# Kernel optimization log

Measured on AMD Instinct MI355X. Metric: run time of the kernel, lower is better.

Reference implementation:

```python
import jax, jax.numpy as jnp
import numpy as np

DEPTH = 2
D_MODEL = 768
D_STATE = 64
EXPAND = 2
D_CONV = 4
D_INNER = EXPAND * D_MODEL          # 1536
DT_RANK = (D_MODEL + 15) // 16      # 48
BATCH, SEQ = 4, 2048


def setup_inputs() -> dict:
    key = jax.random.key(0)
    ks = jax.random.split(key, 8)
    s = 0.02  # small init scale for stability
    return {
        "x": jax.random.normal(ks[0], (BATCH, SEQ, D_MODEL), jnp.float32),
        # per-layer params stacked along leading DEPTH axis
        "in_proj_w": jax.random.normal(ks[1], (DEPTH, 2 * D_INNER, D_MODEL), jnp.float32) * s,
        "conv_w": jax.random.normal(ks[2], (DEPTH, D_INNER, D_CONV), jnp.float32) * s,
        "conv_b": jnp.zeros((DEPTH, D_INNER), jnp.float32),
        "x_proj_w": jax.random.normal(ks[3], (DEPTH, DT_RANK + 2 * D_STATE, D_INNER), jnp.float32) * s,
        "dt_proj_w": jax.random.normal(ks[4], (DEPTH, D_INNER, DT_RANK), jnp.float32) * s,
        "dt_proj_b": jax.random.normal(ks[5], (DEPTH, D_INNER), jnp.float32) * s,
        # S4D-real init: A = -[1..N] per channel -> A_log = log(arange)
        "A_log": jnp.tile(jnp.log(jnp.arange(1, D_STATE + 1, dtype=jnp.float32))[None, None, :],
                          (DEPTH, D_INNER, 1)),
        "D_skip": jnp.ones((DEPTH, D_INNER), jnp.float32),
        "out_proj_w": jax.random.normal(ks[6], (DEPTH, D_MODEL, D_INNER), jnp.float32) * s,
    }


def _causal_conv1d(x, w, b):
    # depthwise causal conv: x [B,L,d], w [d,K], b [d]
    L = x.shape[1]
    xp = jnp.pad(x, ((0, 0), (D_CONV - 1, 0), (0, 0)))
    y = b
    for k in range(D_CONV):
        y = y + xp[:, k:k + L, :] * w[:, k]
    return y


def _selective_scan(u, dt, A, Bm, Cm):
    # u, dt: [B,L,d]; A: [d,N]; Bm, Cm: [B,L,N]
    def step(h, inp):
        dt_t, B_t, C_t, u_t = inp  # [B,d],[B,N],[B,N],[B,d]
        dA = jnp.exp(dt_t[..., None] * A)                         # [B,d,N]
        h = dA * h + dt_t[..., None] * B_t[:, None, :] * u_t[..., None]
        y_t = jnp.einsum('bdn,bn->bd', h, C_t)
        return h, y_t

    h0 = jnp.zeros((u.shape[0], u.shape[2], A.shape[1]), u.dtype)
    xs = (jnp.swapaxes(dt, 0, 1), jnp.swapaxes(Bm, 0, 1),
          jnp.swapaxes(Cm, 0, 1), jnp.swapaxes(u, 0, 1))
    _, ys = jax.lax.scan(step, h0, xs)  # ys [L,B,d]
    return jnp.swapaxes(ys, 0, 1)


def _mamba_layer(x, Wi, cw, cb, Wx, Wdt, bdt, A_log, Dp, Wo):
    xz = x @ Wi.T                                  # [B,L,2*d_inner]
    xpart, z = jnp.split(xz, 2, axis=-1)
    xpart = jax.nn.silu(_causal_conv1d(xpart, cw, cb))
    xdbl = xpart @ Wx.T                            # [B,L,dt_rank+2N]
    dt_in, Bm, Cm = jnp.split(xdbl, [DT_RANK, DT_RANK + D_STATE], axis=-1)
    dt = jax.nn.softplus(dt_in @ Wdt.T + bdt)      # [B,L,d_inner]
    A = -jnp.exp(A_log)                            # [d_inner, N]
    y = _selective_scan(xpart, dt, A, Bm, Cm) + Dp * xpart
    y = y * jax.nn.silu(z)
    return y @ Wo.T                                # [B,L,d_model]


def reference(x, in_proj_w, conv_w, conv_b, x_proj_w, dt_proj_w, dt_proj_b,
              A_log, D_skip, out_proj_w):
    for i in range(DEPTH):
        x = _mamba_layer(x, in_proj_w[i], conv_w[i], conv_b[i], x_proj_w[i],
                         dt_proj_w[i], dt_proj_b[i], A_log[i], D_skip[i],
                         out_proj_w[i])
    return x
```

## Files before the change

kernel.cpp:

```cpp
#include <hip/hip_runtime.h>
#include <hip/hip_bf16.h>
#include <math.h>

#define DEPTH   2
#define DM      768
#define DS      64
#define DC      4
#define DI      1536
#define DTR     48
#define BATCH   4
#define SEQ     2048
#define MROWS   (BATCH*SEQ)
#define XDC     (DTR + 2*DS)
#define NC      8
#define TCH     (SEQ/NC)
#define LOG2E   1.44269504088896f

typedef __attribute__((ext_vector_type(8))) short bf16x8;
typedef __attribute__((ext_vector_type(4))) float f32x4;
typedef __attribute__((ext_vector_type(2))) float f32x2;
typedef __attribute__((ext_vector_type(2))) unsigned int uint2v;
typedef unsigned short ushort_t;
#define GAS __attribute__((address_space(1)))
#define LAS __attribute__((address_space(3)))

__device__ __forceinline__ float silu_fast(float x) {
    return x / (1.f + __expf(-x));
}
__device__ __forceinline__ float softplus_acc(float x) {
    return x > 20.f ? x : log1pf(expf(x));
}

__device__ __forceinline__ ushort_t bf16_hi(float f) {
    unsigned u = __float_as_uint(f);
    unsigned hr = u + 0x7FFF + ((u >> 16) & 1);
    return (ushort_t)(hr >> 16);
}

__device__ __forceinline__ f32x2 merge_x32_2(f32x2 a, f32x2 b) {
#if __has_builtin(__builtin_amdgcn_permlane32_swap)
    const uint2v rx = __builtin_amdgcn_permlane32_swap(
        __float_as_uint(a.x), __float_as_uint(b.x), false, false);
    const uint2v ry = __builtin_amdgcn_permlane32_swap(
        __float_as_uint(a.y), __float_as_uint(b.y), false, false);
    const f32x2 s0 = {__uint_as_float(rx[0]), __uint_as_float(ry[0])};
    const f32x2 s1 = {__uint_as_float(rx[1]), __uint_as_float(ry[1])};
    return s0 + s1;
#else
    const f32x2 sa = {a.x + __shfl_xor(a.x, 32, 64), a.y + __shfl_xor(a.y, 32, 64)};
    const f32x2 sb = {b.x + __shfl_xor(b.x, 32, 64), b.y + __shfl_xor(b.y, 32, 64)};
    return (threadIdx.x & 32) ? sb : sa;
#endif
}

__device__ __forceinline__ f32x2 merge_x16_2(f32x2 a, f32x2 b) {
#if __has_builtin(__builtin_amdgcn_permlane16_swap)
    const uint2v rx = __builtin_amdgcn_permlane16_swap(
        __float_as_uint(a.x), __float_as_uint(b.x), false, false);
    const uint2v ry = __builtin_amdgcn_permlane16_swap(
        __float_as_uint(a.y), __float_as_uint(b.y), false, false);
    const f32x2 s0 = {__uint_as_float(rx[0]), __uint_as_float(ry[0])};
    const f32x2 s1 = {__uint_as_float(rx[1]), __uint_as_float(ry[1])};
    return s0 + s1;
#else
    const f32x2 sa = {a.x + __shfl_xor(a.x, 16, 64), a.y + __shfl_xor(a.y, 16, 64)};
    const f32x2 sb = {b.x + __shfl_xor(b.x, 16, 64), b.y + __shfl_xor(b.y, 16, 64)};
    return (threadIdx.x & 16) ? sb : sa;
#endif
}

template <int CTRL>
__device__ __forceinline__ f32x2 dpp_add2(f32x2 x) {
    const int tx = __builtin_amdgcn_update_dpp(
        0, __float_as_int(x.x), CTRL, 0xF, 0xF, true);
    const int ty = __builtin_amdgcn_update_dpp(
        0, __float_as_int(x.y), CTRL, 0xF, 0xF, true);
    const f32x2 t = {__int_as_float(tx), __int_as_float(ty)};
    return x + t;
}
__device__ __forceinline__ f32x2 rowsum16_2(f32x2 x) {
    x = dpp_add2<0x128>(x);
    x = dpp_add2<0x124>(x);
    x = dpp_add2<0x122>(x);
    x = dpp_add2<0x121>(x);
    return x;
}

__global__ __launch_bounds__(256) void quant_bf16(
    const float* __restrict__ in, ushort_t* __restrict__ hi)
{
    const size_t i = ((size_t)blockIdx.x * 256 + threadIdx.x) * 4;
    const float4 v = *(const float4*)(in + i);
    ushort4 h;
    h.x = bf16_hi(v.x); h.y = bf16_hi(v.y);
    h.z = bf16_hi(v.z); h.w = bf16_hi(v.w);
    *(ushort4*)(hi + i) = h;
}

__global__ __launch_bounds__(256, 2) void gemm_mfma(
    const ushort_t* __restrict__ A, const ushort_t* __restrict__ W,
    float* __restrict__ C, int N, int K, int ldA, int ldW,
    ushort_t* __restrict__ Chi, float4* __restrict__ bc4out, int mode)
{
    __shared__ ushort_t lds[2][128 * 32];
    const int tid  = threadIdx.x;
    const int wave = tid >> 6, lane = tid & 63;

    int bx = blockIdx.x, by = blockIdx.y;
    {
        const int X   = gridDim.x;
        const int fid = by * X + bx;
        const int xcd = fid & 7;
        const int j   = fid >> 3;
        const int jX  = j / X;
        by = xcd * (gridDim.y >> 3) + jX;
        bx = j - jX * X;
    }
    const int bm0 = by * 128, bn0 = bx * 128;
    const int wm = (wave >> 1) * 64, wn = (wave & 1) * 64;

    const int srow = lane >> 2;
    const int skq  = (lane & 3) * 8;

    f32x4 acc[4][4];
#pragma unroll
    for (int i = 0; i < 4; i++)
#pragma unroll
        for (int j = 0; j < 4; j++) acc[i][j] = (f32x4){0.f, 0.f, 0.f, 0.f};

    const int lm  = lane & 15;
    const int kg8 = (lane >> 4) * 8;

    for (int k0 = 0; k0 < K; k0 += 32) {
#pragma unroll
        for (int j = 0; j < 4; j++) {
            const int ldid = wave * 4 + j;
            const int buf  = ldid >> 3;
            const int slot = ldid & 7;
            const ushort_t* gsrc = buf ? W : A;
            const int ldg = buf ? ldW : ldA;
            const int rb  = buf ? bn0 : bm0;
            const ushort_t* ga = gsrc + (size_t)(rb + slot * 16 + srow) * ldg + k0 + skq;
            __builtin_amdgcn_global_load_lds(
                (const GAS unsigned*)ga, (LAS unsigned*)&lds[buf][slot * 512], 16, 0, 0);
        }
        __syncthreads();

        bf16x8 ah[4], bh[4];
#pragma unroll
        for (int i = 0; i < 4; i++) {
            const int ar = (wm + i * 16 + lm) * 32 + kg8;
            ah[i] = *(const bf16x8*)&lds[0][ar];
            const int br = (wn + i * 16 + lm) * 32 + kg8;
            bh[i] = *(const bf16x8*)&lds[1][br];
        }
#pragma unroll
        for (int mi = 0; mi < 4; mi++)
#pragma unroll
            for (int ni = 0; ni < 4; ni++)
                acc[mi][ni] = __builtin_amdgcn_mfma_f32_16x16x32_bf16(
                    ah[mi], bh[ni], acc[mi][ni], 0, 0, 0);
        __syncthreads();
    }

#pragma unroll
    for (int mi = 0; mi < 4; mi++)
#pragma unroll
        for (int ni = 0; ni < 4; ni++) {
            const int rowb = bm0 + wm + mi * 16 + (lane >> 4) * 4;
            const int colg = bn0 + wn + ni * 16 + lm;
            if (mode == 1) {
#pragma unroll
                for (int r = 0; r < 4; r++)
                    Chi[(size_t)(rowb + r) * N + colg] = bf16_hi(acc[mi][ni][r]);
            } else if (mode == 2) {
                if (colg >= DTR && colg < DTR + 2 * DS) {
                    const f32x4 a = acc[mi][ni];
                    bc4out[(size_t)(rowb >> 2) * 128 + (colg - DTR)] =
                        make_float4(a[0], a[1], a[2], a[3]);
                } else if (colg < DTR) {
#pragma unroll
                    for (int r = 0; r < 4; r++)
                        C[(size_t)(rowb + r) * N + colg] = acc[mi][ni][r];
                }
            } else {
#pragma unroll
                for (int r = 0; r < 4; r++)
                    if (colg < N)
                        C[(size_t)(rowb + r) * N + colg] = acc[mi][ni][r];
            }
        }
}

__global__ __launch_bounds__(256, 2) void gemm_dt_T(
    const float* __restrict__ Wdt, const float* __restrict__ xdbl,
    const float* __restrict__ bias, float* __restrict__ dtT)
{
    __shared__ float As[8][132];
    __shared__ float Bs[8][132];
    const int tid = threadIdx.x;
    const int bd0 = blockIdx.y * 128;
    const int bt0 = blockIdx.x * 128;
    const int b   = blockIdx.z;
    const int tx = tid & 15;
    const int ty = tid >> 4;
    const int lrow = tid >> 1;
    const int lk4  = (tid & 1) * 4;

    float acc[8][8];
#pragma unroll
    for (int i = 0; i < 8; i++)
#pragma unroll
        for (int j = 0; j < 8; j++) acc[i][j] = 0.f;

    for (int k0 = 0; k0 < DTR; k0 += 8) {
        const float4 av = *(const float4*)(Wdt + (size_t)(bd0 + lrow) * DTR + k0 + lk4);
        const float4 wv = *(const float4*)(xdbl + ((size_t)b * SEQ + bt0 + lrow) * XDC + k0 + lk4);
        __syncthreads();
        As[lk4 + 0][lrow] = av.x; As[lk4 + 1][lrow] = av.y;
        As[lk4 + 2][lrow] = av.z; As[lk4 + 3][lrow] = av.w;
        Bs[lk4 + 0][lrow] = wv.x; Bs[lk4 + 1][lrow] = wv.y;
        Bs[lk4 + 2][lrow] = wv.z; Bs[lk4 + 3][lrow] = wv.w;
        __syncthreads();
#pragma unroll
        for (int kk = 0; kk < 8; kk++) {
            const float4 a0 = *(const float4*)&As[kk][ty * 8];
            const float4 a1 = *(const float4*)&As[kk][ty * 8 + 4];
            const float4 b0 = *(const float4*)&Bs[kk][tx * 8];
            const float4 b1 = *(const float4*)&Bs[kk][tx * 8 + 4];
            const float ar[8] = {a0.x, a0.y, a0.z, a0.w, a1.x, a1.y, a1.z, a1.w};
            const float br[8] = {b0.x, b0.y, b0.z, b0.w, b1.x, b1.y, b1.z, b1.w};
#pragma unroll
            for (int i = 0; i < 8; i++)
#pragma unroll
                for (int j = 0; j < 8; j++)
                    acc[i][j] = fmaf(ar[i], br[j], acc[i][j]);
        }
    }

#pragma unroll
    for (int i = 0; i < 8; i++) {
        const int d = bd0 + ty * 8 + i;
        const float bb = bias[d];
#pragma unroll
        for (int j4 = 0; j4 < 8; j4 += 4) {
            float4 v = make_float4(acc[i][j4], acc[i][j4 + 1], acc[i][j4 + 2], acc[i][j4 + 3]);
            v.x = softplus_acc(v.x + bb);
            v.y = softplus_acc(v.y + bb);
            v.z = softplus_acc(v.z + bb);
            v.w = softplus_acc(v.w + bb);
            *(float4*)(dtT + ((size_t)b * DI + d) * SEQ + bt0 + tx * 8 + j4) = v;
        }
    }
}

__global__ __launch_bounds__(256) void conv_silu_T2(
    const float* __restrict__ xz, const float* __restrict__ cw,
    const float* __restrict__ cb, float* __restrict__ uT,
    ushort_t* __restrict__ uh)
{
    __shared__ float tin[67][65];
    __shared__ float ttr[64][65];
    const int tid = threadIdx.x;
    const int d0 = blockIdx.x * 64, t0 = blockIdx.y * 64, b = blockIdx.z;
    const int cl = tid & 63, q = tid >> 6;

    for (int r = q; r < 67; r += 4) {
        const int t = t0 - 3 + r;
        float v = 0.f;
        if (t >= 0) v = xz[((size_t)b * SEQ + t) * (2 * DI) + d0 + cl];
        tin[r][cl] = v;
    }
    __syncthreads();

    const float4 w = ((const float4*)cw)[d0 + cl];
    const float bb = cb[d0 + cl];
#pragma unroll
    for (int i = 0; i < 16; i++) {
        const int t = q * 16 + i;
        float a = bb;
        a = fmaf(tin[t + 0][cl], w.x, a);
        a = fmaf(tin[t + 1][cl], w.y, a);
        a = fmaf(tin[t + 2][cl], w.z, a);
        a = fmaf(tin[t + 3][cl], w.w, a);
        a = silu_fast(a);
        ttr[cl][t] = a;
        const size_t row = (size_t)b * SEQ + t0 + t;
        uh[row * DI + d0 + cl] = bf16_hi(a);
    }
    __syncthreads();
#pragma unroll
    for (int i = 0; i < 16; i++) {
        const int d = q * 16 + i;
        uT[((size_t)b * DI + d0 + d) * SEQ + t0 + cl] = ttr[d][cl];
    }
}


#define TAIL_STEP(E, G)                                                \
    {                                                                  \
        const f32x2 dte = {dt0[G].E, dt1[G].E};                        \
        const f32x2 ue  = {u0v[G].E, u1v[G].E};                        \
        const f32x2 w2  = An2 * r2;                                    \
        const f32x2 ee  = {__builtin_amdgcn_exp2f(w2.x),               \
                           __builtin_amdgcn_exp2f(w2.y)};              \
        h2 = h2 + ee * ((dte * ue) * B4[G].E);                         \
        r2 = r2 + dte;                                                 \
    }

__global__ __launch_bounds__(256, 2) void scan_tail(
    const float* __restrict__ dtT, const float* __restrict__ uT,
    const float4* __restrict__ bc4, const float* __restrict__ A_log,
    float* __restrict__ hend)
{
    const int wid  = __builtin_amdgcn_readfirstlane(
                        (int)((blockIdx.x * 256 + threadIdx.x) >> 6));
    const int lane = threadIdx.x & 63;
    const int c   = wid & (NC - 1);
    const int bdq = wid >> 3;
    const int bd0 = bdq * 2;
    const int b   = bd0 / DI;
    const int d0  = bd0 - b * DI;

    const f32x2 An2 = {-expf(A_log[(size_t)d0 * DS + lane]) * LOG2E,
                       -expf(A_log[(size_t)(d0 + 1) * DS + lane]) * LOG2E};
    const float* dtp0 = dtT + (size_t)bd0 * SEQ + c * TCH;
    const float* dtp1 = dtp0 + SEQ;
    const float* up0  = uT  + (size_t)bd0 * SEQ + c * TCH;
    const float* up1  = up0 + SEQ;
    const float4* Bp = bc4 + ((size_t)b * (SEQ / 4) + c * (TCH / 4)) * 128 + lane;

    f32x2 h2 = {0.f, 0.f}, r2 = {0.f, 0.f};
    for (int tb = TCH - 16; tb >= 0; tb -= 16) {
        float4 dt0[4], dt1[4], u0v[4], u1v[4], B4[4];
#pragma unroll
        for (int g = 0; g < 4; g++) {
            dt0[g] = *(const float4*)(dtp0 + tb + 4 * g);
            dt1[g] = *(const float4*)(dtp1 + tb + 4 * g);
            u0v[g] = *(const float4*)(up0 + tb + 4 * g);
            u1v[g] = *(const float4*)(up1 + tb + 4 * g);
            B4[g]  = Bp[(size_t)(tb / 4 + g) * 128];
        }
#pragma unroll
        for (int g = 3; g >= 0; g--) {
            TAIL_STEP(w, g)
            TAIL_STEP(z, g)
            TAIL_STEP(y, g)
            TAIL_STEP(x, g)
        }
        if (__all((An2.x * r2.x < -30.f) && (An2.y * r2.y < -30.f))) break;
    }
    hend[((size_t)bd0 * NC + c) * DS + lane]       = h2.x;
    hend[((size_t)(bd0 + 1) * NC + c) * DS + lane] = h2.y;
}

__global__ __launch_bounds__(256) void scan_phase2(
    const float* __restrict__ dtT, const float* __restrict__ A_log,
    const float* __restrict__ hend, float* __restrict__ h0out)
{
    const int bd   = (blockIdx.x * 256 + threadIdx.x) >> 6;
    const int lane = threadIdx.x & 63;
    const int d    = bd % DI;

    const float* dtp = dtT + (size_t)bd * SEQ + lane * 32;
    float s = 0.f;
#pragma unroll
    for (int g = 0; g < 8; g++) {
        const float4 v = *(const float4*)(dtp + 4 * g);
        s += (v.x + v.y) + (v.z + v.w);
    }
    s += __shfl_xor(s, 1, 64);
    s += __shfl_xor(s, 2, 64);
    s += __shfl_xor(s, 4, 64);

    const float An = -expf(A_log[d * DS + lane]) * LOG2E;
    float h = 0.f;
#pragma unroll
    for (int c = 0; c < NC; c++) {
        const float sdt = __shfl(s, 8 * c, 64);
        const size_t off = ((size_t)bd * NC + c) * DS + lane;
        h0out[off] = h;
        h = fmaf(__builtin_amdgcn_exp2f(An * sdt), h, hend[off]);
    }
}


#define LOAD6(D0, D1, U0, U1, BB_, CC_, TB)                            \
    _Pragma("unroll")                                                  \
    for (int g = 0; g < 4; g++) {                                      \
        D0[g]  = *(const float4*)(dtp0 + (TB) + 4 * g);                \
        D1[g]  = *(const float4*)(dtp1 + (TB) + 4 * g);                \
        U0[g]  = *(const float4*)(up0 + (TB) + 4 * g);                 \
        U1[g]  = *(const float4*)(up1 + (TB) + 4 * g);                 \
        BB_[g] = Bp[(size_t)((TB) / 4 + g) * 128];                     \
        CC_[g] = Cp[(size_t)((TB) / 4 + g) * 128];                     \
    }

#define P3_STEP(E, G, D0, D1, U0, U1, BB_, CC_, LF)                    \
    {                                                                  \
        const f32x2 dte = {D0[G].E, D1[G].E};                          \
        const f32x2 ue  = {U0[G].E, U1[G].E};                          \
        f32x2 w2 = dte * An2;                                          \
        const f32x2 ee = {__builtin_amdgcn_exp2f(w2.x),                \
                          __builtin_amdgcn_exp2f(w2.y)};               \
        const f32x2 p2 = (dte * ue) * BB_[G].E;                        \
        h2 = ee * h2 + p2;                                             \
        LF = h2 * CC_[G].E;                                            \
    }

#define P3_BLOCK(D0, D1, U0, U1, BB_, CC_, TBASE)                      \
    {                                                                  \
        f32x2 m[8];                                                    \
        _Pragma("unroll")                                              \
        for (int g = 0; g < 4; g++) {                                  \
            f32x2 lf0, lf1, lf2, lf3;                                  \
            P3_STEP(x, g, D0, D1, U0, U1, BB_, CC_, lf0)               \
            P3_STEP(y, g, D0, D1, U0, U1, BB_, CC_, lf1)               \
            P3_STEP(z, g, D0, D1, U0, U1, BB_, CC_, lf2)               \
            P3_STEP(w, g, D0, D1, U0, U1, BB_, CC_, lf3)               \
            m[2 * g]     = merge_x32_2(lf0, lf1);                      \
            m[2 * g + 1] = merge_x32_2(lf2, lf3);                      \
        }                                                              \
        const f32x2 q0 = rowsum16_2(merge_x16_2(m[0], m[1]));          \
        const f32x2 q1 = rowsum16_2(merge_x16_2(m[2], m[3]));          \
        const f32x2 q2 = rowsum16_2(merge_x16_2(m[4], m[5]));          \
        const f32x2 q3 = rowsum16_2(merge_x16_2(m[6], m[7]));          \
        const f32x2 v = (lane & 2) ? ((lane & 1) ? q3 : q2)            \
                                   : ((lane & 1) ? q1 : q0);           \
        if ((lane & 15) < 4) {                                         \
            sp0[(TBASE) + wtt] = v.x;                                  \
            sp1[(TBASE) + wtt] = v.y;                                  \
        }                                                              \
    }

__global__ __launch_bounds__(256, 2) void scan_phase3(
    const float* __restrict__ dtT, const float* __restrict__ uT,
    const float4* __restrict__ bc4, const float* __restrict__ A_log,
    const float* __restrict__ hin, float* __restrict__ sX)
{
    const int tid  = threadIdx.x;
    const int wid  = __builtin_amdgcn_readfirstlane(
                        (int)((blockIdx.x * 256 + tid) >> 6));
    const int lane = tid & 63;
    const int c   = wid & (NC - 1);
    const int bdq = wid >> 3;
    const int bd0 = bdq * 2;
    const int b   = bd0 / DI;
    const int d0  = bd0 - b * DI;

    const f32x2 An2 = {-expf(A_log[(size_t)d0 * DS + lane]) * LOG2E,
                       -expf(A_log[(size_t)(d0 + 1) * DS + lane]) * LOG2E};

    const float* dtp0 = dtT + (size_t)bd0 * SEQ + c * TCH;
    const float* dtp1 = dtp0 + SEQ;
    const float* up0  = uT  + (size_t)bd0 * SEQ + c * TCH;
    const float* up1  = up0 + SEQ;
    const float4* Bp = bc4 + ((size_t)b * (SEQ / 4) + c * (TCH / 4)) * 128 + lane;
    const float4* Cp = Bp + 64;

    const size_t L0 = (size_t)bd0 * SEQ + c * TCH;
    const size_t L1 = L0 + SEQ;
    float* sp0 = sX + (L0 / 1536) * 3072 + (L0 % 1536);
    float* sp1 = sX + (L1 / 1536) * 3072 + (L1 % 1536);

    const int wr  = lane >> 4;
    const int wtt = 4 * (lane & 3) + (((wr & 1) << 1) | (wr >> 1));

    f32x2 h2 = {hin[((size_t)bd0 * NC + c) * DS + lane],
                hin[((size_t)(bd0 + 1) * NC + c) * DS + lane]};

    float4 dA0[4], dA1[4], uA0[4], uA1[4], BA4[4], CA4[4];
    float4 dB0[4], dB1[4], uB0[4], uB1[4], BB4[4], CB4[4];
    LOAD6(dA0, dA1, uA0, uA1, BA4, CA4, 0);

    for (int tb = 0; tb < TCH; tb += 32) {
        LOAD6(dB0, dB1, uB0, uB1, BB4, CB4, tb + 16);
        P3_BLOCK(dA0, dA1, uA0, uA1, BA4, CA4, tb);
        LOAD6(dA0, dA1, uA0, uA1, BA4, CA4, tb + 32);
        P3_BLOCK(dB0, dB1, uB0, uB1, BB4, CB4, tb + 16);
    }
}

__global__ __launch_bounds__(256) void gate_split_T(
    const float* __restrict__ xz, const float* __restrict__ uT,
    const float* __restrict__ Dskip, ushort_t* __restrict__ yh)
{
    __shared__ float zt[64][65];
    __shared__ float yt[64][65];
    const int tid = threadIdx.x;
    const int d0 = blockIdx.x * 64, t0 = blockIdx.y * 64, b = blockIdx.z;
    const int cl = tid & 63, q = tid >> 6;
#pragma unroll
    for (int i = 0; i < 16; i++) {
        const int r = q * 16 + i;
        zt[r][cl] = xz[((size_t)b * SEQ + t0 + r) * (2 * DI) + DI + d0 + cl];
    }
    __syncthreads();
#pragma unroll
    for (int i = 0; i < 16; i++) {
        const int dd = q * 16 + i;
        const size_t Lrow = ((size_t)b * DI + d0 + dd) * SEQ + t0;
        const float s = xz[(Lrow / 1536) * 3072 + (Lrow % 1536) + cl];
        const float u = uT[Lrow + cl];
        const float Dd = Dskip[d0 + dd];
        yt[dd][cl] = (s + Dd * u) * silu_fast(zt[cl][dd]);
    }
    __syncthreads();
#pragma unroll
    for (int i = 0; i < 16; i++) {
        const int t = q * 16 + i;
        const size_t row = (size_t)b * SEQ + t0 + t;
        yh[row * DI + d0 + cl] = bf16_hi(yt[cl][t]);
    }
}

extern "C" void kernel_launch(void* const* d_in, const int* in_sizes, int n_in,
                              void* d_out, int out_size, void* d_ws, size_t ws_size,
                              hipStream_t stream) {
    (void)in_sizes; (void)n_in; (void)out_size; (void)ws_size;
    const float* x    = (const float*)d_in[0];
    const float* Wi   = (const float*)d_in[1];
    const float* cw   = (const float*)d_in[2];
    const float* cb   = (const float*)d_in[3];
    const float* Wx   = (const float*)d_in[4];
    const float* Wdt  = (const float*)d_in[5];
    const float* bdt  = (const float*)d_in[6];
    const float* Alog = (const float*)d_in[7];
    const float* Dsk  = (const float*)d_in[8];
    const float* Wo   = (const float*)d_in[9];
    float* out = (float*)d_out;

    float* xz    = (float*)d_ws;
    float* uT    = xz    + (size_t)MROWS * (2 * DI);
    float* dtT   = uT    + (size_t)MROWS * DI;
    float* xdbl  = dtT   + (size_t)MROWS * DI;
    float* bcT   = xdbl  + (size_t)MROWS * XDC;
    float* xnext = bcT   + (size_t)BATCH * 128 * SEQ;
    float* hend  = xnext;
    float* h0buf = xnext + (size_t)BATCH * DI * NC * DS;

    ushort_t* sh  = (ushort_t*)uT;
    ushort_t* wih = (ushort_t*)(dtT + (size_t)MROWS * DM);
    ushort_t* uh  = (ushort_t*)dtT;
    ushort_t* wxh = (ushort_t*)xnext;
    ushort_t* woh = (ushort_t*)xdbl;
    ushort_t* yh  = (ushort_t*)xnext;

    for (int i = 0; i < DEPTH; i++) {
        const float* Wi_l   = Wi   + (size_t)i * 2 * DI * DM;
        const float* cw_l   = cw   + (size_t)i * DI * DC;
        const float* cb_l   = cb   + (size_t)i * DI;
        const float* Wx_l   = Wx   + (size_t)i * XDC * DI;
        const float* Wdt_l  = Wdt  + (size_t)i * DI * DTR;
        const float* bdt_l  = bdt  + (size_t)i * DI;
        const float* Alog_l = Alog + (size_t)i * DI * DS;
        const float* Dsk_l  = Dsk  + (size_t)i * DI;
        const float* Wo_l   = Wo   + (size_t)i * DM * DI;

        if (i == 0)
            quant_bf16<<<(size_t)MROWS * DM / 1024, 256, 0, stream>>>(x, sh);
        quant_bf16<<<(size_t)2 * DI * DM / 1024, 256, 0, stream>>>(Wi_l, wih);
        gemm_mfma<<<dim3(2 * DI / 128, MROWS / 128), 256, 0, stream>>>(
            sh, wih, xz, 2 * DI, DM, DM, DM, nullptr, nullptr, 0);
        conv_silu_T2<<<dim3(DI / 64, SEQ / 64, BATCH), 256, 0, stream>>>(
            xz, cw_l, cb_l, uT, uh);
        quant_bf16<<<(size_t)XDC * DI / 1024, 256, 0, stream>>>(Wx_l, wxh);
        gemm_mfma<<<dim3((XDC + 127) / 128, MROWS / 128), 256, 0, stream>>>(
            uh, wxh, xdbl, XDC, DI, DI, DI, nullptr, (float4*)bcT, 2);
        gemm_dt_T<<<dim3(SEQ / 128, DI / 128, BATCH), 256, 0, stream>>>(
            Wdt_l, xdbl, bdt_l, dtT);
        scan_tail<<<(BATCH * DI * NC) / 8, 256, 0, stream>>>(
            dtT, uT, (const float4*)bcT, Alog_l, hend);
        scan_phase2<<<(BATCH * DI) / 4, 256, 0, stream>>>(
            dtT, Alog_l, hend, h0buf);
        scan_phase3<<<(BATCH * DI * NC) / 8, 256, 0, stream>>>(
            dtT, uT, (const float4*)bcT, Alog_l, h0buf, xz);
        gate_split_T<<<dim3(DI / 64, SEQ / 64, BATCH), 256, 0, stream>>>(
            xz, uT, Dsk_l, yh);
        quant_bf16<<<(size_t)DM * DI / 1024, 256, 0, stream>>>(Wo_l, woh);
        if (i == DEPTH - 1)
            gemm_mfma<<<dim3(DM / 128, MROWS / 128), 256, 0, stream>>>(
                yh, woh, out, DM, DI, DI, DI, nullptr, nullptr, 0);
        else
            gemm_mfma<<<dim3(DM / 128, MROWS / 128), 256, 0, stream>>>(
                yh, woh, nullptr, DM, DI, DI, DI, sh, nullptr, 1);
    }
}
```

Before: 1.094 ms.

## Fuse scan chunk-tail and carry-propagation kernels; merge weight quant launches

The per-chunk tail scan and the phase-2 carry propagation are merged into one kernel in which each wave walks all eight chunks of its channel pair, keeps the chunk-end states and dt sums in registers, and writes the initial states directly. This removes the hend round trip through memory and one launch. Once a chunk's decay has underflowed, the remaining steps only sum dt. The trade-off is 8x fewer waves, each with a longer serial loop, which reduces parallelism in the scan tail. Separately, the Wi and Wx bf16 quantisation launches are combined into one kernel.

```diff
diff --git a/kernel.cpp b/kernel.cpp
--- a/kernel.cpp
+++ b/kernel.cpp
@@ -97,6 +97,26 @@
     *(ushort4*)(hi + i) = h;
 }
 
+#define WI_BLKS (2 * DI * DM / 1024)
+#define WX_BLKS (XDC * DI / 1024)
+__global__ __launch_bounds__(256) void quant_w2(
+    const float* __restrict__ Wi, const float* __restrict__ Wx,
+    ushort_t* __restrict__ wih, ushort_t* __restrict__ wxh)
+{
+    const int blk = blockIdx.x;
+    const float* src;
+    ushort_t* dst;
+    size_t base;
+    if (blk < WI_BLKS) { src = Wi; dst = wih; base = (size_t)blk * 1024; }
+    else               { src = Wx; dst = wxh; base = (size_t)(blk - WI_BLKS) * 1024; }
+    const size_t i = base + (size_t)threadIdx.x * 4;
+    const float4 v = *(const float4*)(src + i);
+    ushort4 h;
+    h.x = bf16_hi(v.x); h.y = bf16_hi(v.y);
+    h.z = bf16_hi(v.z); h.w = bf16_hi(v.w);
+    *(ushort4*)(dst + i) = h;
+}
+
 __global__ __launch_bounds__(256, 2) void gemm_mfma(
     const ushort_t* __restrict__ A, const ushort_t* __restrict__ W,
     float* __restrict__ C, int N, int K, int ldA, int ldW,
@@ -308,79 +328,82 @@
         r2 = r2 + dte;                                                 \
     }
 
-__global__ __launch_bounds__(256, 2) void scan_tail(
+__global__ __launch_bounds__(256, 2) void scan_tail2(
     const float* __restrict__ dtT, const float* __restrict__ uT,
     const float4* __restrict__ bc4, const float* __restrict__ A_log,
-    float* __restrict__ hend)
+    float* __restrict__ h0out)
 {
     const int wid  = __builtin_amdgcn_readfirstlane(
                         (int)((blockIdx.x * 256 + threadIdx.x) >> 6));
     const int lane = threadIdx.x & 63;
-    const int c   = wid & (NC - 1);
-    const int bdq = wid >> 3;
+    const int bdq = wid;
     const int bd0 = bdq * 2;
     const int b   = bd0 / DI;
     const int d0  = bd0 - b * DI;
 
     const f32x2 An2 = {-expf(A_log[(size_t)d0 * DS + lane]) * LOG2E,
                        -expf(A_log[(size_t)(d0 + 1) * DS + lane]) * LOG2E};
-    const float* dtp0 = dtT + (size_t)bd0 * SEQ + c * TCH;
-    const float* dtp1 = dtp0 + SEQ;
-    const float* up0  = uT  + (size_t)bd0 * SEQ + c * TCH;
-    const float* up1  = up0 + SEQ;
-    const float4* Bp = bc4 + ((size_t)b * (SEQ / 4) + c * (TCH / 4)) * 128 + lane;
-
-    f32x2 h2 = {0.f, 0.f}, r2 = {0.f, 0.f};
-    for (int tb = TCH - 16; tb >= 0; tb -= 16) {
-        float4 dt0[4], dt1[4], u0v[4], u1v[4], B4[4];
-#pragma unroll
-        for (int g = 0; g < 4; g++) {
-            dt0[g] = *(const float4*)(dtp0 + tb + 4 * g);
-            dt1[g] = *(const float4*)(dtp1 + tb + 4 * g);
-            u0v[g] = *(const float4*)(up0 + tb + 4 * g);
-            u1v[g] = *(const float4*)(up1 + tb + 4 * g);
-            B4[g]  = Bp[(size_t)(tb / 4 + g) * 128];
+    const float* dtb0 = dtT + (size_t)bd0 * SEQ;
+    const float* dtb1 = dtb0 + SEQ;
+    const float* ub0  = uT  + (size_t)bd0 * SEQ;
+    const float* ub1  = ub0 + SEQ;
+    const float4* Bb  = bc4 + (size_t)b * (SEQ / 4) * 128 + lane;
+
+    f32x2 hend_c[NC], sdt_c[NC];
+#pragma unroll
+    for (int c = 0; c < NC; c++) {
+        const float* dtp0 = dtb0 + c * TCH;
+        const float* dtp1 = dtb1 + c * TCH;
+        const float* up0  = ub0 + c * TCH;
+        const float* up1  = ub1 + c * TCH;
+        const float4* Bp  = Bb + (size_t)c * (TCH / 4) * 128;
+
+        f32x2 h2 = {0.f, 0.f}, r2 = {0.f, 0.f};
+        int tb = TCH - 16;
+        for (; tb >= 0; tb -= 16) {
+            float4 dt0[4], dt1[4], u0v[4], u1v[4], B4[4];
+#pragma unroll
+            for (int g = 0; g < 4; g++) {
+                dt0[g] = *(const float4*)(dtp0 + tb + 4 * g);
+                dt1[g] = *(const float4*)(dtp1 + tb + 4 * g);
+                u0v[g] = *(const float4*)(up0 + tb + 4 * g);
+                u1v[g] = *(const float4*)(up1 + tb + 4 * g);
+                B4[g]  = Bp[(size_t)(tb / 4 + g) * 128];
+            }
+#pragma unroll
+            for (int g = 3; g >= 0; g--) {
+                TAIL_STEP(w, g)
+                TAIL_STEP(z, g)
+                TAIL_STEP(y, g)
+                TAIL_STEP(x, g)
+            }
+            if (__all((An2.x * r2.x < -30.f) && (An2.y * r2.y < -30.f))) {
+                tb -= 16;
+                break;
+            }
         }
-#pragma unroll
-        for (int g = 3; g >= 0; g--) {
-            TAIL_STEP(w, g)
-            TAIL_STEP(z, g)
-            TAIL_STEP(y, g)
-            TAIL_STEP(x, g)
+        for (; tb >= 0; tb -= 16) {
+            float4 dt0[4], dt1[4];
+#pragma unroll
+            for (int g = 0; g < 4; g++) {
+                dt0[g] = *(const float4*)(dtp0 + tb + 4 * g);
+                dt1[g] = *(const float4*)(dtp1 + tb + 4 * g);
+                r2.x += (dt0[g].x + dt0[g].y) + (dt0[g].z + dt0[g].w);
+                r2.y += (dt1[g].x + dt1[g].y) + (dt1[g].z + dt1[g].w);
+            }
         }
-        if (__all((An2.x * r2.x < -30.f) && (An2.y * r2.y < -30.f))) break;
-    }
-    hend[((size_t)bd0 * NC + c) * DS + lane]       = h2.x;
-    hend[((size_t)(bd0 + 1) * NC + c) * DS + lane] = h2.y;
-}
-
-__global__ __launch_bounds__(256) void scan_phase2(
-    const float* __restrict__ dtT, const float* __restrict__ A_log,
-    const float* __restrict__ hend, float* __restrict__ h0out)
-{
-    const int bd   = (blockIdx.x * 256 + threadIdx.x) >> 6;
-    const int lane = threadIdx.x & 63;
-    const int d    = bd % DI;
-
-    const float* dtp = dtT + (size_t)bd * SEQ + lane * 32;
-    float s = 0.f;
-#pragma unroll
-    for (int g = 0; g < 8; g++) {
-        const float4 v = *(const float4*)(dtp + 4 * g);
-        s += (v.x + v.y) + (v.z + v.w);
-    }
-    s += __shfl_xor(s, 1, 64);
-    s += __shfl_xor(s, 2, 64);
-    s += __shfl_xor(s, 4, 64);
-
-    const float An = -expf(A_log[d * DS + lane]) * LOG2E;
-    float h = 0.f;
+        hend_c[c] = h2;
+        sdt_c[c] = r2;
+    }
+
+    f32x2 h = {0.f, 0.f};
 #pragma unroll
     for (int c = 0; c < NC; c++) {
-        const float sdt = __shfl(s, 8 * c, 64);
-        const size_t off = ((size_t)bd * NC + c) * DS + lane;
-        h0out[off] = h;
-        h = fmaf(__builtin_amdgcn_exp2f(An * sdt), h, hend[off]);
+        h0out[((size_t)bd0 * NC + c) * DS + lane]       = h.x;
+        h0out[((size_t)(bd0 + 1) * NC + c) * DS + lane] = h.y;
+        const f32x2 e = {__builtin_amdgcn_exp2f(An2.x * sdt_c[c].x),
+                         __builtin_amdgcn_exp2f(An2.y * sdt_c[c].y)};
+        h = e * h + hend_c[c];
     }
 }
 
@@ -536,13 +559,12 @@
     float* xdbl  = dtT   + (size_t)MROWS * DI;
     float* bcT   = xdbl  + (size_t)MROWS * XDC;
     float* xnext = bcT   + (size_t)BATCH * 128 * SEQ;
-    float* hend  = xnext;
-    float* h0buf = xnext + (size_t)BATCH * DI * NC * DS;
+    float* h0buf = xnext;
 
     ushort_t* sh  = (ushort_t*)uT;
     ushort_t* wih = (ushort_t*)(dtT + (size_t)MROWS * DM);
     ushort_t* uh  = (ushort_t*)dtT;
-    ushort_t* wxh = (ushort_t*)xnext;
+    ushort_t* wxh = (ushort_t*)(xnext + (size_t)BATCH * DI * NC * DS);
     ushort_t* woh = (ushort_t*)xdbl;
     ushort_t* yh  = (ushort_t*)xnext;
 
@@ -559,20 +581,17 @@
 
         if (i == 0)
             quant_bf16<<<(size_t)MROWS * DM / 1024, 256, 0, stream>>>(x, sh);
-        quant_bf16<<<(size_t)2 * DI * DM / 1024, 256, 0, stream>>>(Wi_l, wih);
+        quant_w2<<<WI_BLKS + WX_BLKS, 256, 0, stream>>>(Wi_l, Wx_l, wih, wxh);
         gemm_mfma<<<dim3(2 * DI / 128, MROWS / 128), 256, 0, stream>>>(
             sh, wih, xz, 2 * DI, DM, DM, DM, nullptr, nullptr, 0);
         conv_silu_T2<<<dim3(DI / 64, SEQ / 64, BATCH), 256, 0, stream>>>(
             xz, cw_l, cb_l, uT, uh);
-        quant_bf16<<<(size_t)XDC * DI / 1024, 256, 0, stream>>>(Wx_l, wxh);
         gemm_mfma<<<dim3((XDC + 127) / 128, MROWS / 128), 256, 0, stream>>>(
             uh, wxh, xdbl, XDC, DI, DI, DI, nullptr, (float4*)bcT, 2);
         gemm_dt_T<<<dim3(SEQ / 128, DI / 128, BATCH), 256, 0, stream>>>(
             Wdt_l, xdbl, bdt_l, dtT);
-        scan_tail<<<(BATCH * DI * NC) / 8, 256, 0, stream>>>(
-            dtT, uT, (const float4*)bcT, Alog_l, hend);
-        scan_phase2<<<(BATCH * DI) / 4, 256, 0, stream>>>(
-            dtT, Alog_l, hend, h0buf);
+        scan_tail2<<<(BATCH * DI / 2) / 4, 256, 0, stream>>>(
+            dtT, uT, (const float4*)bcT, Alog_l, h0buf);
         scan_phase3<<<(BATCH * DI * NC) / 8, 256, 0, stream>>>(
             dtT, uT, (const float4*)bcT, Alog_l, h0buf, xz);
         gate_split_T<<<dim3(DI / 64, SEQ / 64, BATCH), 256, 0, stream>>>(
```

After: 1.154 ms. 5.5% more time.
